# Performance work log

Measured on AMD Instinct MI355X. Metric: run time of the kernel, lower is better.

The kernel has to match this reference:

```python
import jax, jax.numpy as jnp
import numpy as np

B, L, F, H, U = 512, 64, 2048, 512, 512


def setup_inputs() -> dict:
    key = jax.random.key(0)
    ks = jax.random.split(key, 10)
    s = 0.05
    return {
        'features': jax.random.normal(ks[0], (B, L, F), jnp.float32),
        'hidden': jax.random.normal(ks[1], (B, H), jnp.float32),
        'W1': jax.random.normal(ks[2], (F, U), jnp.float32) * s,
        'b1': jnp.zeros((U,), jnp.float32),
        'W2': jax.random.normal(ks[3], (H, U), jnp.float32) * s,
        'b2': jnp.zeros((U,), jnp.float32),
        'V': jax.random.normal(ks[4], (U, 1), jnp.float32) * s,
        'bV': jnp.zeros((1,), jnp.float32),
        'W3': jax.random.normal(ks[5], (F + H, U), jnp.float32) * s,
        'b3': jnp.zeros((U,), jnp.float32),
        'ka1': jax.random.normal(ks[6], (H, L), jnp.float32) * s,
        'kb1': jax.random.normal(ks[7], (L, L), jnp.float32) * s,
        'ka2': jax.random.normal(ks[8], (H, L), jnp.float32) * s,
        'kb2': jax.random.normal(ks[9], (L, L), jnp.float32) * s,
    }


def reference(features, hidden, W1, b1, W2, b2, V, bV, W3, b3, ka1, kb1, ka2, kb2):
    # features: [B, L, F], hidden: [B, H]
    Lp = features.shape[1]
    h = hidden[:, None, :]  # [B, 1, H] = hidden_with_time_axis

    # score_model == 'default'
    score = jnp.tanh(features @ W1 + b1 + (h @ W2 + b2))  # [B, L, U]
    logits = score @ V + bV  # [B, L, 1]
    attention_weights = jax.nn.softmax(logits, axis=1)  # [B, L, 1]

    # local_att == 'True': Gaussian window re-weighting (vectorized version of
    # the original nested Python loops over (batch, position)).
    def local_p(ka, kb):
        t = jnp.tanh(h @ ka) @ kb  # [B, 1, L]
        t = jax.nn.sigmoid(t) * jnp.sqrt(jnp.float32(Lp))
        return jnp.transpose(t, (0, 2, 1))  # [B, L, 1]

    p1 = local_p(ka1, kb1)  # predicted row center, [B, L, 1]
    p2 = local_p(ka2, kb2)  # predicted col center, [B, L, 1]

    i = jnp.arange(Lp, dtype=jnp.float32)
    g = jnp.sqrt(jnp.float32(Lp))
    rows = jnp.floor((i + 1.0) / g)                 # s_t[..., 0]
    cols = jnp.floor(jnp.mod(i + 1.0, g)) - 1.0     # s_t[..., 1]
    d2 = (rows[None, :, None] - p1) ** 2 + (cols[None, :, None] - p2) ** 2  # [B, L, 1]

    D = 1.0
    attention_weights = attention_weights * jnp.exp(-d2 / (0.5 * D * D))

    context_vector = jnp.sum(attention_weights * features, axis=1)  # [B, F]

    # context_vector_concat == 'True'
    out = jnp.tanh(jnp.concatenate([context_vector, hidden], axis=-1)) @ W3 + b3  # [B, U]
    return out, attention_weights
```

## Files before the change

kernel.cpp:

```cpp
#include <hip/hip_runtime.h>

typedef __bf16 bf16x8 __attribute__((ext_vector_type(8)));
typedef float f32x4 __attribute__((ext_vector_type(4)));

static __device__ __forceinline__ unsigned short f2bf(float f) {
  union { float fv; unsigned u; } v; v.fv = f;
  unsigned u = v.u;
  u += 0x7fffu + ((u >> 16) & 1u);
  return (unsigned short)(u >> 16);
}

static __device__ __forceinline__ float fast_tanh(float x) {
  x = fminf(fmaxf(x, -15.f), 15.f);
  float ex = __expf(2.f * x);
  return (ex - 1.f) / (ex + 1.f);
}

__global__ __launch_bounds__(256) void pack_all(
    const float* __restrict__ W1, const float* __restrict__ W2,
    const float* __restrict__ W3,
    unsigned short* __restrict__ W1p, unsigned short* __restrict__ W2p,
    unsigned short* __restrict__ W3p) {
  __shared__ float tile[32][65];
  const int N = 512;
  const float* W; unsigned short* P; int nk;
  if (blockIdx.z == 0)      { W = W1; P = W1p; nk = 64; }
  else if (blockIdx.z == 1) { W = W2; P = W2p; nk = 16; }
  else                      { W = W3; P = W3p; nk = 80; }
  if ((int)blockIdx.x >= nk) return;
  int k0 = blockIdx.x * 32, n0 = blockIdx.y * 64;
  int t = threadIdx.x;
  int nn = t & 63, kkb = t >> 6;
#pragma unroll
  for (int i = 0; i < 8; ++i) {
    int kk = kkb + i * 4;
    tile[kk][nn] = W[(size_t)(k0 + kk) * N + n0 + nn];
  }
  __syncthreads();
#pragma unroll
  for (int i = 0; i < 8; ++i) {
    int e = t + i * 256;
    int k8 = e & 7, n = (e >> 3) & 63, c = e >> 9;
    size_t dst = (size_t)((k0 >> 3) + c) * 4096 + (size_t)(n0 + n) * 8 + k8;
    P[dst] = f2bf(tile[c * 8 + k8][n]);
  }
}

__global__ __launch_bounds__(128) void prep_batch(
    const float* __restrict__ hidden,
    const float* __restrict__ ka1, const float* __restrict__ kb1,
    const float* __restrict__ ka2, const float* __restrict__ kb2,
    float* __restrict__ gauss,
    unsigned short* __restrict__ hid_bf,
    unsigned short* __restrict__ A2) {
  int b = blockIdx.x, t = threadIdx.x;
  __shared__ float hl[512];
  __shared__ float tt[128];
  __shared__ float pp[128];
  for (int i = t; i < 512; i += 128) {
    float v = hidden[b * 512 + i];
    hl[i] = v;
    hid_bf[b * 512 + i] = f2bf(v);
    A2[(size_t)b * 2560 + 2048 + i] = f2bf(tanhf(v));
  }
  __syncthreads();
  {
    const float* ka = (t < 64) ? ka1 : ka2;
    int lp = t & 63;
    float s0 = 0.f, s1 = 0.f, s2 = 0.f, s3 = 0.f;
    for (int h = 0; h < 512; h += 4) {
      s0 += hl[h + 0] * ka[(h + 0) * 64 + lp];
      s1 += hl[h + 1] * ka[(h + 1) * 64 + lp];
      s2 += hl[h + 2] * ka[(h + 2) * 64 + lp];
      s3 += hl[h + 3] * ka[(h + 3) * 64 + lp];
    }
    tt[t] = tanhf((s0 + s1) + (s2 + s3));
  }
  __syncthreads();
  {
    const float* kb = (t < 64) ? kb1 : kb2;
    const float* ts = (t < 64) ? tt : tt + 64;
    int l = t & 63;
    float s = 0.f;
    for (int j = 0; j < 64; ++j) s += ts[j] * kb[j * 64 + l];
    pp[t] = 8.0f / (1.0f + expf(-s));
  }
  __syncthreads();
  if (t < 64) {
    float fi = (float)(t + 1);
    float r = floorf(fi * 0.125f);
    float c = floorf(fmodf(fi, 8.0f)) - 1.0f;
    float dr = r - pp[t], dc = c - pp[64 + t];
    gauss[b * 64 + t] = expf(-2.0f * (dr * dr + dc * dc));
  }
}

__global__ __launch_bounds__(256, 4) void gemm64d(
    const unsigned short* __restrict__ A, int lda, int k8_stride, int nsteps,
    const unsigned short* __restrict__ Wp,
    const float* __restrict__ bias,
    float* __restrict__ C) {
  __shared__ unsigned short lA[64 * 40];
  int m0 = blockIdx.x * 64, n0 = blockIdx.y * 64;
  int z = blockIdx.z;
  int k8 = z * k8_stride;
  int t = threadIdx.x;
  int w = t >> 6, lane = t & 63, q = lane >> 4, l15 = lane & 15;
  f32x4 acc[4] = {};
  int arow = t >> 2, achk = (t & 3) * 8;
  const unsigned short* pA = A + (size_t)(m0 + arow) * lda + (size_t)k8 * 8 + achk;
  const unsigned short* pB = Wp + ((size_t)(k8 + q) * 512 + n0 + w * 16 + l15) * 8;
  int4 av = *(const int4*)(pA);
  int4 bv = *(const int4*)(pB);
  for (int ks = 0; ks < nsteps; ++ks) {
    __syncthreads();
    *(int4*)(lA + arow * 40 + achk) = av;
    __syncthreads();
    int ksn = (ks + 1 < nsteps) ? ks + 1 : ks;
    av = *(const int4*)(pA + ksn * 32);
    int4 bn = *(const int4*)(pB + (size_t)ksn * 16384);
    bf16x8 bf = *(const bf16x8*)&bv;
#pragma unroll
    for (int mt = 0; mt < 4; ++mt) {
      bf16x8 af = *(const bf16x8*)(lA + (mt * 16 + l15) * 40 + q * 8);
      acc[mt] = __builtin_amdgcn_mfma_f32_16x16x32_bf16(af, bf, acc[mt], 0, 0, 0);
    }
    bv = bn;
  }
  int col = n0 + w * 16 + l15;
  if (bias) {
    float bsv = bias[col];
#pragma unroll
    for (int mt = 0; mt < 4; ++mt)
#pragma unroll
      for (int j = 0; j < 4; ++j)
        C[(size_t)(m0 + mt * 16 + q * 4 + j) * 512 + col] = acc[mt][j] + bsv;
  } else {
    float* Cp = C + (size_t)z * 262144;
#pragma unroll
    for (int mt = 0; mt < 4; ++mt)
#pragma unroll
      for (int j = 0; j < 4; ++j)
        Cp[(size_t)(m0 + mt * 16 + q * 4 + j) * 512 + col] = acc[mt][j];
  }
}

__global__ __launch_bounds__(256) void reduce4(const float* __restrict__ part,
                                               const float* __restrict__ b3,
                                               float* __restrict__ out) {
  int i = blockIdx.x * 256 + threadIdx.x;
  int base = i * 4;
  int n = base & 511;
  float4 p0 = *(const float4*)(part + base);
  float4 p1 = *(const float4*)(part + 262144 + base);
  float4 p2 = *(const float4*)(part + 524288 + base);
  float4 p3 = *(const float4*)(part + 786432 + base);
  float4 bv = *(const float4*)(b3 + n);
  float4 r;
  r.x = p0.x + p1.x + p2.x + p3.x + bv.x;
  r.y = p0.y + p1.y + p2.y + p3.y + bv.y;
  r.z = p0.z + p1.z + p2.z + p3.z + bv.z;
  r.w = p0.w + p1.w + p2.w + p3.w + bv.w;
  *(float4*)(out + base) = r;
}

__global__ __launch_bounds__(256, 2) void attn_main(
    const float* __restrict__ feat,
    const unsigned short* __restrict__ W1p,
    const float* __restrict__ b1,
    const float* __restrict__ hb,
    const float* __restrict__ V,
    const float* __restrict__ bVp,
    const float* __restrict__ gauss,
    float* __restrict__ aw_out,
    unsigned short* __restrict__ A2) {
  __shared__ unsigned short lA[2][64 * 40];
  __shared__ float red[64 * 4];
  __shared__ float awl[64];
  int b = blockIdx.x, t = threadIdx.x;
  int w = t >> 6, lane = t & 63, q = lane >> 4, l15 = lane & 15;
  f32x4 acc[4][8] = {};
  int row0 = t >> 3, ch0 = t & 7;
  const float* Ab = feat + (size_t)b * (64 * 2048);
  const float* pA0 = Ab + row0 * 2048 + ch0 * 4;
  const float* pA1 = pA0 + 32 * 2048;
  const unsigned short* pB = W1p + ((size_t)q * 512 + w * 128 + l15) * 8;
  int wA = row0 * 40 + ch0 * 4;

  float vv[8], bb[8];
#pragma unroll
  for (int nt = 0; nt < 8; ++nt) {
    int u = w * 128 + nt * 16 + l15;
    vv[nt] = V[u];
    bb[nt] = b1[u] + hb[b * 512 + u];
  }
  float gs = (t < 64) ? gauss[b * 64 + t] : 0.f;
  float bV0 = bVp[0];

  auto mmaStep = [&](int buf, const int4* B) {
#pragma unroll
    for (int mt = 0; mt < 4; ++mt) {
      bf16x8 af = *(const bf16x8*)(&lA[buf][(mt * 16 + l15) * 40 + q * 8]);
#pragma unroll
      for (int nt = 0; nt < 8; ++nt)
        acc[mt][nt] = __builtin_amdgcn_mfma_f32_16x16x32_bf16(
            af, *(const bf16x8*)&B[nt], acc[mt][nt], 0, 0, 0);
    }
  };
  auto stage = [&](int buf, const float4& x0, const float4& x1) {
    ushort4 u0, u1;
    u0.x = f2bf(x0.x); u0.y = f2bf(x0.y); u0.z = f2bf(x0.z); u0.w = f2bf(x0.w);
    u1.x = f2bf(x1.x); u1.y = f2bf(x1.y); u1.z = f2bf(x1.z); u1.w = f2bf(x1.w);
    *(ushort4*)(&lA[buf][wA]) = u0;
    *(ushort4*)(&lA[buf][wA + 1280]) = u1;
  };

  int4 bc[8], bn[8];
  float4 a0, a1, na0, na1;
  a0 = *(const float4*)(pA0);
  a1 = *(const float4*)(pA1);
#pragma unroll
  for (int nt = 0; nt < 8; ++nt) bc[nt] = *(const int4*)(pB + nt * 128);
  stage(0, a0, a1);
  na0 = *(const float4*)(pA0 + 32);
  na1 = *(const float4*)(pA1 + 32);
#pragma unroll
  for (int nt = 0; nt < 8; ++nt) bn[nt] = *(const int4*)(pB + 16384 + nt * 128);
  __syncthreads();

  for (int s2 = 0; s2 < 32; ++s2) {
    int s = 2 * s2;
    stage(1, na0, na1);
    {
      int kf = (s + 2 < 64) ? s + 2 : 63;
      a0 = *(const float4*)(pA0 + kf * 32);
      a1 = *(const float4*)(pA1 + kf * 32);
    }
    mmaStep(0, bc);
    {
      int kf = (s + 2 < 64) ? s + 2 : 63;
      const unsigned short* bp = pB + (size_t)kf * 16384;
#pragma unroll
      for (int nt = 0; nt < 8; ++nt) bc[nt] = *(const int4*)(bp + nt * 128);
    }
    __syncthreads();
    stage(0, a0, a1);
    {
      int kf = (s + 3 < 64) ? s + 3 : 63;
      na0 = *(const float4*)(pA0 + kf * 32);
      na1 = *(const float4*)(pA1 + kf * 32);
    }
    mmaStep(1, bn);
    {
      int kf = (s + 3 < 64) ? s + 3 : 63;
      const unsigned short* bp = pB + (size_t)kf * 16384;
#pragma unroll
      for (int nt = 0; nt < 8; ++nt) bn[nt] = *(const int4*)(bp + nt * 128);
    }
    __syncthreads();
  }

#pragma unroll
  for (int mt = 0; mt < 4; ++mt) {
#pragma unroll
    for (int j = 0; j < 4; ++j) {
      float p = 0.f;
#pragma unroll
      for (int nt = 0; nt < 8; ++nt)
        p += fast_tanh(acc[mt][nt][j] + bb[nt]) * vv[nt];
      p += __shfl_xor(p, 1);
      p += __shfl_xor(p, 2);
      p += __shfl_xor(p, 4);
      p += __shfl_xor(p, 8);
      if (l15 == 0) red[(mt * 16 + q * 4 + j) * 4 + w] = p;
    }
  }
  __syncthreads();
  if (t < 64) {
    float s = bV0 + red[t * 4] + red[t * 4 + 1] + red[t * 4 + 2] + red[t * 4 + 3];
    float mx = s;
#pragma unroll
    for (int o = 1; o < 64; o <<= 1) mx = fmaxf(mx, __shfl_xor(mx, o));
    float e = __expf(s - mx);
    float sm = e;
#pragma unroll
    for (int o = 1; o < 64; o <<= 1) sm += __shfl_xor(sm, o);
    float a = (e / sm) * gs;
    awl[t] = a;
    aw_out[b * 64 + t] = a;
  }
  __syncthreads();
  float4 c0 = make_float4(0.f, 0.f, 0.f, 0.f);
  float4 c1 = make_float4(0.f, 0.f, 0.f, 0.f);
  const float* pF = Ab + t * 8;
  for (int l = 0; l < 64; ++l) {
    float a = awl[l];
    float4 f0 = *(const float4*)(pF + l * 2048);
    float4 f1 = *(const float4*)(pF + l * 2048 + 4);
    c0.x += a * f0.x; c0.y += a * f0.y; c0.z += a * f0.z; c0.w += a * f0.w;
    c1.x += a * f1.x; c1.y += a * f1.y; c1.z += a * f1.z; c1.w += a * f1.w;
  }
  ushort4 o0, o1;
  o0.x = f2bf(fast_tanh(c0.x)); o0.y = f2bf(fast_tanh(c0.y));
  o0.z = f2bf(fast_tanh(c0.z)); o0.w = f2bf(fast_tanh(c0.w));
  o1.x = f2bf(fast_tanh(c1.x)); o1.y = f2bf(fast_tanh(c1.y));
  o1.z = f2bf(fast_tanh(c1.z)); o1.w = f2bf(fast_tanh(c1.w));
  *(ushort4*)(A2 + (size_t)b * 2560 + t * 8) = o0;
  *(ushort4*)(A2 + (size_t)b * 2560 + t * 8 + 4) = o1;
}

extern "C" void kernel_launch(void* const* d_in, const int* in_sizes, int n_in,
                              void* d_out, int out_size, void* d_ws, size_t ws_size,
                              hipStream_t stream) {
  (void)in_sizes; (void)n_in; (void)out_size; (void)ws_size;
  const float* feat   = (const float*)d_in[0];
  const float* hidden = (const float*)d_in[1];
  const float* W1  = (const float*)d_in[2];
  const float* b1  = (const float*)d_in[3];
  const float* W2  = (const float*)d_in[4];
  const float* b2  = (const float*)d_in[5];
  const float* V   = (const float*)d_in[6];
  const float* bV  = (const float*)d_in[7];
  const float* W3  = (const float*)d_in[8];
  const float* b3  = (const float*)d_in[9];
  const float* ka1 = (const float*)d_in[10];
  const float* kb1 = (const float*)d_in[11];
  const float* ka2 = (const float*)d_in[12];
  const float* kb2 = (const float*)d_in[13];

  char* ws = (char*)d_ws;
  unsigned short* W3p   = (unsigned short*)(ws);
  unsigned short* A2    = (unsigned short*)(ws + 2621440);
  unsigned short* W1p   = (unsigned short*)(ws + 5242880);
  unsigned short* W2p   = (unsigned short*)(ws + 7340032);
  unsigned short* hidbf = (unsigned short*)(ws + 7864320);
  float*          hb    = (float*)(ws + 8388608);
  float*          gauss = (float*)(ws + 9437184);
  float*          part  = (float*)(ws + 5242880);

  float* out    = (float*)d_out;
  float* aw_out = out + 512 * 512;

  pack_all<<<dim3(80, 8, 3), 256, 0, stream>>>(W1, W2, W3, W1p, W2p, W3p);
  prep_batch<<<512, 128, 0, stream>>>(hidden, ka1, kb1, ka2, kb2, gauss, hidbf, A2);
  gemm64d<<<dim3(8, 8, 1), 256, 0, stream>>>(hidbf, 512, 0, 16, W2p, b2, hb);
  attn_main<<<512, 256, 0, stream>>>(feat, W1p, b1, hb, V, bV, gauss, aw_out, A2);
  gemm64d<<<dim3(8, 8, 4), 256, 0, stream>>>(A2, 2560, 80, 20, W3p, nullptr, part);
  reduce4<<<256, 256, 0, stream>>>(part, b3, out);
}
```

Before: 507.8 us.

## Restructure GEMM main loops with double-buffered LDS and wider K steps

The fused attention kernel now stages 64-wide K slices (16 floats per thread) into a double-buffered LDS tile, so it runs 32 iterations of two MFMA K-halves instead of 64 single-K iterations. This halves the number of barriers, and the B fragments for both halves are loaded up front. The generic gemm64d kernel becomes double-buffered with one barrier per step instead of two, and its occupancy hint drops from 4 to 2. The context loop gets an unroll-4 hint. The cost is higher register pressure from 16 B fragments plus 4 float4 prefetches, and the B loads are no longer prefetched a full step ahead.

```diff
diff --git a/kernel.cpp b/kernel.cpp
--- a/kernel.cpp
+++ b/kernel.cpp
@@ -8,6 +8,13 @@
   unsigned u = v.u;
   u += 0x7fffu + ((u >> 16) & 1u);
   return (unsigned short)(u >> 16);
+}
+
+static __device__ __forceinline__ int4 pack8(const float4& x0, const float4& x1) {
+  union { unsigned short u[8]; int4 v; } r;
+  r.u[0] = f2bf(x0.x); r.u[1] = f2bf(x0.y); r.u[2] = f2bf(x0.z); r.u[3] = f2bf(x0.w);
+  r.u[4] = f2bf(x1.x); r.u[5] = f2bf(x1.y); r.u[6] = f2bf(x1.z); r.u[7] = f2bf(x1.w);
+  return r.v;
 }
 
 static __device__ __forceinline__ float fast_tanh(float x) {
@@ -95,12 +102,12 @@
   }
 }
 
-__global__ __launch_bounds__(256, 4) void gemm64d(
+__global__ __launch_bounds__(256, 2) void gemm64d(
     const unsigned short* __restrict__ A, int lda, int k8_stride, int nsteps,
     const unsigned short* __restrict__ Wp,
     const float* __restrict__ bias,
     float* __restrict__ C) {
-  __shared__ unsigned short lA[64 * 40];
+  __shared__ unsigned short lA[2][64 * 40];
   int m0 = blockIdx.x * 64, n0 = blockIdx.y * 64;
   int z = blockIdx.z;
   int k8 = z * k8_stride;
@@ -110,22 +117,23 @@
   int arow = t >> 2, achk = (t & 3) * 8;
   const unsigned short* pA = A + (size_t)(m0 + arow) * lda + (size_t)k8 * 8 + achk;
   const unsigned short* pB = Wp + ((size_t)(k8 + q) * 512 + n0 + w * 16 + l15) * 8;
-  int4 av = *(const int4*)(pA);
-  int4 bv = *(const int4*)(pB);
+  *(int4*)(&lA[0][arow * 40 + achk]) = *(const int4*)(pA);
+  __syncthreads();
   for (int ks = 0; ks < nsteps; ++ks) {
+    int p = ks & 1;
+    int4 bv = *(const int4*)(pB + (size_t)ks * 16384);
+    int ksn = (ks < nsteps - 1) ? ks + 1 : ks;
+    int4 av = *(const int4*)(pA + ksn * 32);
+    bf16x8 af[4];
+#pragma unroll
+    for (int mt = 0; mt < 4; ++mt)
+      af[mt] = *(const bf16x8*)(&lA[p][(mt * 16 + l15) * 40 + q * 8]);
+    bf16x8 bf = *(const bf16x8*)&bv;
+#pragma unroll
+    for (int mt = 0; mt < 4; ++mt)
+      acc[mt] = __builtin_amdgcn_mfma_f32_16x16x32_bf16(af[mt], bf, acc[mt], 0, 0, 0);
+    *(int4*)(&lA[1 - p][arow * 40 + achk]) = av;
     __syncthreads();
-    *(int4*)(lA + arow * 40 + achk) = av;
-    __syncthreads();
-    int ksn = (ks + 1 < nsteps) ? ks + 1 : ks;
-    av = *(const int4*)(pA + ksn * 32);
-    int4 bn = *(const int4*)(pB + (size_t)ksn * 16384);
-    bf16x8 bf = *(const bf16x8*)&bv;
-#pragma unroll
-    for (int mt = 0; mt < 4; ++mt) {
-      bf16x8 af = *(const bf16x8*)(lA + (mt * 16 + l15) * 40 + q * 8);
-      acc[mt] = __builtin_amdgcn_mfma_f32_16x16x32_bf16(af, bf, acc[mt], 0, 0, 0);
-    }
-    bv = bn;
   }
   int col = n0 + w * 16 + l15;
   if (bias) {
@@ -174,18 +182,17 @@
     const float* __restrict__ gauss,
     float* __restrict__ aw_out,
     unsigned short* __restrict__ A2) {
-  __shared__ unsigned short lA[2][64 * 40];
+  __shared__ unsigned short lA[2][64 * 72];
   __shared__ float red[64 * 4];
   __shared__ float awl[64];
   int b = blockIdx.x, t = threadIdx.x;
   int w = t >> 6, lane = t & 63, q = lane >> 4, l15 = lane & 15;
   f32x4 acc[4][8] = {};
-  int row0 = t >> 3, ch0 = t & 7;
+  int arow = t >> 2, aseg = (t & 3) * 16;
   const float* Ab = feat + (size_t)b * (64 * 2048);
-  const float* pA0 = Ab + row0 * 2048 + ch0 * 4;
-  const float* pA1 = pA0 + 32 * 2048;
+  const float* pA = Ab + (size_t)arow * 2048 + aseg;
   const unsigned short* pB = W1p + ((size_t)q * 512 + w * 128 + l15) * 8;
-  int wA = row0 * 40 + ch0 * 4;
+  int wA = arow * 72 + aseg;
 
   float vv[8], bb[8];
 #pragma unroll
@@ -197,82 +204,61 @@
   float gs = (t < 64) ? gauss[b * 64 + t] : 0.f;
   float bV0 = bVp[0];
 
-  auto mmaStep = [&](int buf, const int4* B) {
-#pragma unroll
-    for (int mt = 0; mt < 4; ++mt) {
-      bf16x8 af = *(const bf16x8*)(&lA[buf][(mt * 16 + l15) * 40 + q * 8]);
+  {
+    float4 x0 = *(const float4*)(pA + 0);
+    float4 x1 = *(const float4*)(pA + 4);
+    float4 x2 = *(const float4*)(pA + 8);
+    float4 x3 = *(const float4*)(pA + 12);
+    *(int4*)(&lA[0][wA])     = pack8(x0, x1);
+    *(int4*)(&lA[0][wA + 8]) = pack8(x2, x3);
+  }
+  __syncthreads();
+
+  for (int s = 0; s < 32; ++s) {
+    int p = s & 1;
+    const unsigned short* bp = pB + (size_t)s * 32768;
+    int4 bfr[16];
+#pragma unroll
+    for (int i = 0; i < 16; ++i)
+      bfr[i] = *(const int4*)(bp + (i >> 3) * 16384 + (i & 7) * 128);
+    int sn = (s < 31) ? s + 1 : 31;
+    const float* pn = pA + sn * 64;
+    float4 x0 = *(const float4*)(pn + 0);
+    float4 x1 = *(const float4*)(pn + 4);
+    float4 x2 = *(const float4*)(pn + 8);
+    float4 x3 = *(const float4*)(pn + 12);
+    bf16x8 af[4][2];
+#pragma unroll
+    for (int mt = 0; mt < 4; ++mt)
+#pragma unroll
+      for (int kh = 0; kh < 2; ++kh)
+        af[mt][kh] = *(const bf16x8*)(&lA[p][(mt * 16 + l15) * 72 + kh * 32 + q * 8]);
+#pragma unroll
+    for (int kh = 0; kh < 2; ++kh)
+#pragma unroll
+      for (int mt = 0; mt < 4; ++mt)
+#pragma unroll
+        for (int nt = 0; nt < 8; ++nt)
+          acc[mt][nt] = __builtin_amdgcn_mfma_f32_16x16x32_bf16(
+              af[mt][kh], *(const bf16x8*)&bfr[kh * 8 + nt], acc[mt][nt], 0, 0, 0);
+    *(int4*)(&lA[1 - p][wA])     = pack8(x0, x1);
+    *(int4*)(&lA[1 - p][wA + 8]) = pack8(x2, x3);
+    __syncthreads();
+  }
+
+#pragma unroll
+  for (int mt = 0; mt < 4; ++mt) {
+#pragma unroll
+    for (int j = 0; j < 4; ++j) {
+      float pv = 0.f;
 #pragma unroll
       for (int nt = 0; nt < 8; ++nt)
-        acc[mt][nt] = __builtin_amdgcn_mfma_f32_16x16x32_bf16(
-            af, *(const bf16x8*)&B[nt], acc[mt][nt], 0, 0, 0);
-    }
-  };
-  auto stage = [&](int buf, const float4& x0, const float4& x1) {
-    ushort4 u0, u1;
-    u0.x = f2bf(x0.x); u0.y = f2bf(x0.y); u0.z = f2bf(x0.z); u0.w = f2bf(x0.w);
-    u1.x = f2bf(x1.x); u1.y = f2bf(x1.y); u1.z = f2bf(x1.z); u1.w = f2bf(x1.w);
-    *(ushort4*)(&lA[buf][wA]) = u0;
-    *(ushort4*)(&lA[buf][wA + 1280]) = u1;
-  };
-
-  int4 bc[8], bn[8];
-  float4 a0, a1, na0, na1;
-  a0 = *(const float4*)(pA0);
-  a1 = *(const float4*)(pA1);
-#pragma unroll
-  for (int nt = 0; nt < 8; ++nt) bc[nt] = *(const int4*)(pB + nt * 128);
-  stage(0, a0, a1);
-  na0 = *(const float4*)(pA0 + 32);
-  na1 = *(const float4*)(pA1 + 32);
-#pragma unroll
-  for (int nt = 0; nt < 8; ++nt) bn[nt] = *(const int4*)(pB + 16384 + nt * 128);
-  __syncthreads();
-
-  for (int s2 = 0; s2 < 32; ++s2) {
-    int s = 2 * s2;
-    stage(1, na0, na1);
-    {
-      int kf = (s + 2 < 64) ? s + 2 : 63;
-      a0 = *(const float4*)(pA0 + kf * 32);
-      a1 = *(const float4*)(pA1 + kf * 32);
-    }
-    mmaStep(0, bc);
-    {
-      int kf = (s + 2 < 64) ? s + 2 : 63;
-      const unsigned short* bp = pB + (size_t)kf * 16384;
-#pragma unroll
-      for (int nt = 0; nt < 8; ++nt) bc[nt] = *(const int4*)(bp + nt * 128);
-    }
-    __syncthreads();
-    stage(0, a0, a1);
-    {
-      int kf = (s + 3 < 64) ? s + 3 : 63;
-      na0 = *(const float4*)(pA0 + kf * 32);
-      na1 = *(const float4*)(pA1 + kf * 32);
-    }
-    mmaStep(1, bn);
-    {
-      int kf = (s + 3 < 64) ? s + 3 : 63;
-      const unsigned short* bp = pB + (size_t)kf * 16384;
-#pragma unroll
-      for (int nt = 0; nt < 8; ++nt) bn[nt] = *(const int4*)(bp + nt * 128);
-    }
-    __syncthreads();
-  }
-
-#pragma unroll
-  for (int mt = 0; mt < 4; ++mt) {
-#pragma unroll
-    for (int j = 0; j < 4; ++j) {
-      float p = 0.f;
-#pragma unroll
-      for (int nt = 0; nt < 8; ++nt)
-        p += fast_tanh(acc[mt][nt][j] + bb[nt]) * vv[nt];
-      p += __shfl_xor(p, 1);
-      p += __shfl_xor(p, 2);
-      p += __shfl_xor(p, 4);
-      p += __shfl_xor(p, 8);
-      if (l15 == 0) red[(mt * 16 + q * 4 + j) * 4 + w] = p;
+        pv += fast_tanh(acc[mt][nt][j] + bb[nt]) * vv[nt];
+      pv += __shfl_xor(pv, 1);
+      pv += __shfl_xor(pv, 2);
+      pv += __shfl_xor(pv, 4);
+      pv += __shfl_xor(pv, 8);
+      if (l15 == 0) red[(mt * 16 + q * 4 + j) * 4 + w] = pv;
     }
   }
   __syncthreads();
@@ -293,6 +279,7 @@
   float4 c0 = make_float4(0.f, 0.f, 0.f, 0.f);
   float4 c1 = make_float4(0.f, 0.f, 0.f, 0.f);
   const float* pF = Ab + t * 8;
+#pragma unroll 4
   for (int l = 0; l < 64; ++l) {
     float a = awl[l];
     float4 f0 = *(const float4*)(pF + l * 2048);
```

Result: slower. 525.3 us (+3.4%).
